# Kernel optimization log

Measured on AMD Instinct MI355X. Metric: run time of the kernel, lower is better.

## Reference

```python
import jax, jax.numpy as jnp
import numpy as np


def _log_g(x):
    # numerically stable log of g(x) = where(x>=0, x+0.5, sigmoid(x))
    return jnp.where(x >= 0, jnp.log(jax.nn.relu(x) + 0.5), -jax.nn.softplus(-x))


def setup_inputs() -> dict:
    key = jax.random.key(0)
    k1, k2, k3, k4 = jax.random.split(key, 4)
    B, T, D = 4, 4096, 1024
    Di = 2 * D  # dim_inner = int(dim * expansion_factor), expansion_factor = 2.0
    x = jax.random.normal(k1, (B, T, D), dtype=jnp.float32)
    prev_hidden = jax.random.uniform(k2, (B, Di), dtype=jnp.float32)  # positive carry state
    # torch Linear(dim, 2*dim_inner, bias=False): stored here pre-transposed as [D, 2*Di]
    W_hg = jax.random.normal(k3, (D, 2 * Di), dtype=jnp.float32) * (1.0 / np.sqrt(D))
    # out_proj Linear(dim_inner, dim, bias=False): stored pre-transposed as [Di, D]
    W_out = jax.random.normal(k4, (Di, D), dtype=jnp.float32) * (1.0 / np.sqrt(Di))
    return {"x": x, "prev_hidden": prev_hidden, "W_hg": W_hg, "W_out": W_out}


def reference(x, prev_hidden, W_hg, W_out):
    # x: [B, T, D]; prev_hidden: [B, Di] (positive)
    T = x.shape[1]
    hg = jnp.einsum('btd,de->bte', x, W_hg)          # [B, T, 2*Di]
    hidden, gate = jnp.split(hg, 2, axis=-1)          # each [B, T, Di]

    # Heinsen log-space affine scan: h_t = (1 - z_t) * h_{t-1} + z_t * g(hidden_t)
    log_coeffs = -jax.nn.softplus(gate)               # log(1 - sigmoid(gate))
    log_values = -jax.nn.softplus(-gate) + _log_g(hidden)  # log(sigmoid(gate)) + log g(hidden)

    # prepend carry state
    prev_log = jnp.clip(jnp.log(jnp.clip(prev_hidden, 1e-8, None)), -30.0, None)[:, None]  # [B,1,Di]
    log_values = jnp.concatenate([prev_log, log_values], axis=1)      # [B, T+1, Di]
    log_coeffs = jnp.pad(log_coeffs, ((0, 0), (1, 0), (0, 0)))        # [B, T+1, Di]

    a_star = jnp.cumsum(log_coeffs, axis=1)
    h = jnp.exp(a_star + jax.lax.cumlogsumexp(log_values - a_star, axis=1))  # [B, T+1, Di]
    h = h[:, -T:]                                     # drop carry slot

    next_hidden = h[:, -1]                            # [B, Di]
    out = jnp.einsum('bte,ed->btd', h, W_out)         # [B, T, D]
    return (out, next_hidden)
```

## Files before the change

### kernel.cpp

```cpp
#include <hip/hip_runtime.h>
#include <cstdio>

#define T_LEN 4096
#define B_SZ  4
#define D_IN  1024
#define DI    2048
#define MM    16384
#define NC2   128
#define CHL2  32

typedef __attribute__((ext_vector_type(8))) __bf16 bf16x8;
typedef __attribute__((ext_vector_type(4))) float  f32x4;
typedef __attribute__((ext_vector_type(8))) unsigned short u16x8;

__device__ __forceinline__ unsigned short f2bf(float f){
  unsigned u = __builtin_bit_cast(unsigned, f);
  u += 0x7fffu + ((u >> 16) & 1u);
  return (unsigned short)(u >> 16);
}
__device__ __forceinline__ float bf2f_lo(unsigned u){
  return __builtin_bit_cast(float, u << 16);
}
__device__ __forceinline__ float bf2f_hi(unsigned u){
  return __builtin_bit_cast(float, u & 0xffff0000u);
}
__device__ __forceinline__ float bf2f_s(unsigned short s){
  return __builtin_bit_cast(float, (unsigned)s << 16);
}

__device__ __forceinline__ void async16(void* lds, const void* g){
  __builtin_amdgcn_global_load_lds((const __attribute__((address_space(1))) void*)g,
                                   (__attribute__((address_space(3))) void*)lds, 16, 0, 0);
}

template<int PERM>
__device__ __forceinline__ void transpose_body(const float* __restrict__ src,
                                               unsigned short* __restrict__ dst,
                                               int n0, int k0, int SK, int SN,
                                               float (*tile)[65], int tid){
  #pragma unroll
  for(int it=0; it<16; it++){
    int idx = it*256 + tid;
    int kk = idx>>6, nn = idx&63;
    int n = n0+nn;
    int col = PERM ? (((n>>5)<<4) + (n&15) + ((n&16)?2048:0)) : n;
    tile[kk][nn] = src[(size_t)(k0+kk)*SN + col];
  }
  __syncthreads();
  #pragma unroll
  for(int it=0; it<16; it++){
    int idx = it*256 + tid;
    int nn = idx>>6, kk = idx&63;
    dst[(size_t)(n0+nn)*SK + k0+kk] = f2bf(tile[kk][nn]);
  }
}

__global__ __launch_bounds__(256) void k_prep(const float* __restrict__ x,
                                              unsigned short* __restrict__ xb,
                                              const float* __restrict__ Whg,
                                              unsigned short* __restrict__ wt,
                                              const float* __restrict__ Wout,
                                              unsigned short* __restrict__ wo){
  __shared__ float tile[64][65];
  int bid = blockIdx.x, tid = threadIdx.x;
  if(bid < 8192){
    size_t t = (size_t)bid*256 + tid;
    const float4* xi = (const float4*)x;
    float4 a = xi[2*t], b = xi[2*t+1];
    u16x8 o;
    o[0]=f2bf(a.x); o[1]=f2bf(a.y); o[2]=f2bf(a.z); o[3]=f2bf(a.w);
    o[4]=f2bf(b.x); o[5]=f2bf(b.y); o[6]=f2bf(b.z); o[7]=f2bf(b.w);
    ((u16x8*)xb)[t] = o;
  } else if(bid < 9216){
    int j = bid - 8192;
    transpose_body<1>(Whg, wt, (j&63)*64, (j>>6)*64, 1024, 4096, tile, tid);
  } else {
    int j = bid - 9216;
    transpose_body<0>(Wout, wo, (j&15)*64, (j>>4)*64, 2048, 1024, tile, tid);
  }
}

template<int EPI>
__global__ __launch_bounds__(256, 2)
void k_gemm(const unsigned short* __restrict__ A, const unsigned short* __restrict__ Bt,
            float* __restrict__ C0, unsigned* __restrict__ U0,
            unsigned* __restrict__ U1, unsigned short* __restrict__ Ap,
            unsigned short* __restrict__ Vp, int M, int N, int K){
  __shared__ unsigned short lsA[128*64];
  __shared__ unsigned short lsB[128*64];
  int tid  = threadIdx.x;
  int lane = tid & 63, wave = tid >> 6;
  int wm = wave >> 1, wn = wave & 1;
  int cl = lane & 15, quad = lane >> 4;
  int m0 = blockIdx.y * 128, n0 = blockIdx.x * 128;

  f32x4 acc[4][4];
  #pragma unroll
  for(int i=0;i<4;i++)
    #pragma unroll
    for(int j=0;j<4;j++) acc[i][j] = (f32x4){0.f,0.f,0.f,0.f};

  int g = (tid&7) ^ ((tid>>3)&7);
  const unsigned short* gA = A  + (size_t)(m0 + (tid>>3))*K + g*8;
  const unsigned short* gB = Bt + (size_t)(n0 + (tid>>3))*K + g*8;
  unsigned short* dA = lsA + tid*8;
  unsigned short* dB = lsB + tid*8;

  for(int k0=0; k0<K; k0+=64){
    #pragma unroll
    for(int it=0; it<4; it++){
      async16(dA + it*2048, gA + (size_t)(it*32)*K + k0);
      async16(dB + it*2048, gB + (size_t)(it*32)*K + k0);
    }
    __syncthreads();
    #pragma unroll
    for(int kh=0; kh<2; kh++){
      bf16x8 fa[4], fb[4];
      int sl = ((kh<<2)|quad);
      #pragma unroll
      for(int t2=0;t2<4;t2++){
        int ra = wm*64 + t2*16 + cl;
        int rb = wn*64 + t2*16 + cl;
        fa[t2] = *(const bf16x8*)&lsA[ra*64 + (sl^(cl&7))*8];
        fb[t2] = *(const bf16x8*)&lsB[rb*64 + (sl^(cl&7))*8];
      }
      #pragma unroll
      for(int i=0;i<4;i++)
        #pragma unroll
        for(int j=0;j<4;j++)
          acc[i][j] = __builtin_amdgcn_mfma_f32_16x16x32_bf16(fa[i], fb[j], acc[i][j], 0, 0, 0);
    }
    __syncthreads();
  }

  if(EPI==0){
    #pragma unroll
    for(int i=0;i<4;i++)
      #pragma unroll
      for(int j=0;j<4;j++){
        int n = n0 + wn*64 + j*16 + cl;
        #pragma unroll
        for(int r=0;r<4;r++){
          int m = m0 + wm*64 + i*16 + quad*4 + r;
          C0[(size_t)m*N + n] = acc[i][j][r];
        }
      }
  } else {
    float* lA_f = (float*)lsA;
    float* lV_f = (float*)lsB;
    int ibase = ((n0 + wn*64) >> 1) + cl;
    int odd = cl & 1;
    #pragma unroll
    for(int i=0;i<4;i++)
      #pragma unroll
      for(int p=0;p<2;p++){
        f32x4 hh = acc[i][2*p], gg = acc[i][2*p+1];
        int ii = ibase + p*16;
        float pa = 1.f, pv = 0.f;
        #pragma unroll
        for(int r=0;r<4;r++){
          int m = m0 + wm*64 + i*16 + quad*4 + r;
          float gate = gg[r], hid = hh[r];
          float e  = __expf(gate);
          float cc = 1.f/(1.f + e);
          float z  = (gate > 80.f) ? 1.f : e*cc;
          float gv = (hid >= 0.f) ? (hid + 0.5f) : (1.f/(1.f + __expf(-hid)));
          float vv = z*gv;
          float ccp = __shfl_xor(cc, 1, 64);
          float vvp = __shfl_xor(vv, 1, 64);
          unsigned wlo = odd ? (unsigned)f2bf(vvp) : (unsigned)f2bf(cc);
          unsigned whi = odd ? (unsigned)f2bf(vv)  : (unsigned)f2bf(ccp);
          unsigned* dst = odd ? U1 : U0;
          dst[((size_t)m*DI + (ii & ~1)) >> 1] = wlo | (whi << 16);
          pa *= cc;
          pv = fmaf(cc, pv, vv);
        }
        int seg = wm*16 + i*4 + quad;
        int chl = wn*32 + p*16 + cl;
        lA_f[seg*64 + chl] = pa;
        lV_f[seg*64 + chl] = pv;
      }
    __syncthreads();
    {
      int ch = tid & 63, q = tid >> 6;
      float Ac = 1.f, Vc = 0.f;
      #pragma unroll
      for(int s=0; s<8; s++){
        int idx = (q*8 + s)*64 + ch;
        float a = lA_f[idx], v = lV_f[idx];
        Ac *= a;
        Vc = fmaf(a, Vc, v);
      }
      int b = m0 >> 12;
      int ch32 = ((m0 & 4095) >> 5) + q;
      size_t o = (size_t)(b*NC2 + ch32)*DI + (n0 >> 1) + ch;
      Ap[o] = f2bf(Ac); Vp[o] = f2bf(Vc);
    }
  }
}

__global__ __launch_bounds__(256) void k_scanB(const float* __restrict__ prev,
                                               unsigned short* __restrict__ Ap,
                                               const unsigned short* __restrict__ Vp){
  int t = blockIdx.x*256 + threadIdx.x;
  int i = t & (DI-1); int b = t >> 11;
  float h = fmaxf(prev[t], 1e-8f);
  for(int ch=0; ch<NC2; ch++){
    size_t o = (size_t)(b*NC2 + ch)*DI + i;
    float a = bf2f_s(Ap[o]), vv = bf2f_s(Vp[o]);
    Ap[o] = f2bf(h);
    h = fmaf(a, h, vv);
  }
}

__global__ __launch_bounds__(256) void k_scanC(const unsigned* __restrict__ cp,
                                               unsigned* __restrict__ vp,
                                               const unsigned* __restrict__ hinp,
                                               float* __restrict__ nh){
  int t = blockIdx.x*256 + threadIdx.x;
  int i2 = t & (DI/2 - 1);
  int ch = (t >> 10) & (NC2-1);
  int b  = t >> 17;
  size_t base = ((size_t)(b*T_LEN + ch*CHL2))*(DI/2) + i2;
  unsigned hp = hinp[(size_t)(b*NC2 + ch)*(DI/2) + i2];
  float h0 = bf2f_lo(hp), h1 = bf2f_hi(hp);
  #pragma unroll 4
  for(int s=0; s<CHL2; s++){
    unsigned cu = cp[base], vu = vp[base];
    h0 = fmaf(bf2f_lo(cu), h0, bf2f_lo(vu));
    h1 = fmaf(bf2f_hi(cu), h1, bf2f_hi(vu));
    vp[base] = (unsigned)f2bf(h0) | ((unsigned)f2bf(h1) << 16);
    base += DI/2;
  }
  if(ch == NC2-1){ nh[b*DI + 2*i2] = h0; nh[b*DI + 2*i2 + 1] = h1; }
}

extern "C" void kernel_launch(void* const* d_in, const int* in_sizes, int n_in,
                              void* d_out, int out_size, void* d_ws, size_t ws_size,
                              hipStream_t stream){
  const float* x    = (const float*)d_in[0];
  const float* prev = (const float*)d_in[1];
  const float* Whg  = (const float*)d_in[2];
  const float* Wout = (const float*)d_in[3];
  float* out = (float*)d_out;
  float* nh  = out + (size_t)MM*D_IN;

  const size_t NEED = 117440512;
  if(ws_size < NEED){
    fprintf(stderr, "kernel_launch: ws_size=%zu < needed %zu — aborting launch\n",
            ws_size, NEED);
    return;
  }
  char* ws = (char*)d_ws;
  unsigned short* xb = (unsigned short*)(ws);
  unsigned short* wt = (unsigned short*)(ws + 33554432);
  unsigned short* wo = (unsigned short*)(ws + 41943040);
  unsigned short* v  = (unsigned short*)(ws + 46137344);
  unsigned short* Ap = (unsigned short*)(ws + 113246208);
  unsigned short* Vp = (unsigned short*)(ws + 115343360);
  unsigned* c = (unsigned*)d_out;

  k_prep<<<9728, 256, 0, stream>>>(x, xb, Whg, wt, Wout, wo);

  k_gemm<1><<<dim3(32,128), 256, 0, stream>>>(xb, wt, nullptr, c, (unsigned*)v,
                                              Ap, Vp, MM, 2*DI, D_IN);

  k_scanB<<<32,   256, 0, stream>>>(prev, Ap, Vp);
  k_scanC<<<2048, 256, 0, stream>>>((const unsigned*)c, (unsigned*)v,
                                    (const unsigned*)Ap, nh);

  k_gemm<0><<<dim3(8,128), 256, 0, stream>>>(v, wo, out, nullptr, nullptr,
                                             nullptr, nullptr, MM, D_IN, DI);
}
```

Before: 422.4 us.

## Rewrite GEMM with 256x256 tiles, 4-stage async LDS pipeline and block swizzle

The bf16 MFMA GEMM moves from 128x128 tiles with 256 threads and a single-buffered K=64 loop to 256x256 tiles with 512 threads. K advances in steps of 32 through a 4-deep ring of LDS buffers, with loads issued three stages ahead and guarded by manual vmcnt waits and barriers. It also remaps workgroups for L2 locality and raises wave priority around the MFMA bursts. The aim is to hide global-load latency and raise data reuse. The costs are much more LDS per block, more registers for the accumulators, which can limit occupancy, and fragile hand-written synchronisation.

```diff
diff --git a/kernel.cpp b/kernel.cpp
--- a/kernel.cpp
+++ b/kernel.cpp
@@ -32,6 +32,9 @@
   __builtin_amdgcn_global_load_lds((const __attribute__((address_space(1))) void*)g,
                                    (__attribute__((address_space(3))) void*)lds, 16, 0, 0);
 }
+
+#define BARRIER()    asm volatile("s_barrier" ::: "memory")
+#define VMCNT_BAR(n) asm volatile("s_waitcnt vmcnt(" #n ")\n\ts_barrier" ::: "memory")
 
 template<int PERM>
 __device__ __forceinline__ void transpose_body(const float* __restrict__ src,
@@ -81,68 +84,110 @@
 }
 
 template<int EPI>
-__global__ __launch_bounds__(256, 2)
+__global__ __launch_bounds__(512, 2)
 void k_gemm(const unsigned short* __restrict__ A, const unsigned short* __restrict__ Bt,
             float* __restrict__ C0, unsigned* __restrict__ U0,
             unsigned* __restrict__ U1, unsigned short* __restrict__ Ap,
             unsigned short* __restrict__ Vp, int M, int N, int K){
-  __shared__ unsigned short lsA[128*64];
-  __shared__ unsigned short lsB[128*64];
+  __shared__ __align__(16) unsigned short lsA[4*8192];
+  __shared__ __align__(16) unsigned short lsB[4*8192];
   int tid  = threadIdx.x;
   int lane = tid & 63, wave = tid >> 6;
-  int wm = wave >> 1, wn = wave & 1;
+  int wm = wave >> 2, wn = wave & 3;
   int cl = lane & 15, quad = lane >> 4;
-  int m0 = blockIdx.y * 128, n0 = blockIdx.x * 128;
-
-  f32x4 acc[4][4];
+
+  int gx = gridDim.x;
+  int nwg = gx * gridDim.y;
+  int orig = blockIdx.y * gx + blockIdx.x;
+  int swz = (orig & 7) * (nwg >> 3) + (orig >> 3);
+  int bx = swz % gx, by = swz / gx;
+  int m0 = by * 256, n0 = bx * 256;
+
+  f32x4 acc[8][4];
   #pragma unroll
-  for(int i=0;i<4;i++)
+  for(int i=0;i<8;i++)
     #pragma unroll
     for(int j=0;j<4;j++) acc[i][j] = (f32x4){0.f,0.f,0.f,0.f};
 
-  int g = (tid&7) ^ ((tid>>3)&7);
-  const unsigned short* gA = A  + (size_t)(m0 + (tid>>3))*K + g*8;
-  const unsigned short* gB = Bt + (size_t)(n0 + (tid>>3))*K + g*8;
-  unsigned short* dA = lsA + tid*8;
-  unsigned short* dB = lsB + tid*8;
-
-  for(int k0=0; k0<K; k0+=64){
-    #pragma unroll
-    for(int it=0; it<4; it++){
-      async16(dA + it*2048, gA + (size_t)(it*32)*K + k0);
-      async16(dB + it*2048, gB + (size_t)(it*32)*K + k0);
+  const unsigned short* gA = A  + (size_t)(m0 + (tid>>2))*K + (tid&3)*8;
+  const unsigned short* gB = Bt + (size_t)(n0 + (tid>>2))*K + (tid&3)*8;
+  unsigned short* dA0 = lsA + tid*8;
+  unsigned short* dB0 = lsB + tid*8;
+  const size_t rK = (size_t)128*K;
+
+  int NU = K >> 5;
+
+  #pragma unroll
+  for(int w0=0; w0<3; ++w0){
+    int sw = w0*8192;
+    async16(dA0 + sw,        gA + (size_t)w0*32);
+    async16(dA0 + sw + 4096, gA + rK + (size_t)w0*32);
+    async16(dB0 + sw,        gB + (size_t)w0*32);
+    async16(dB0 + sw + 4096, gB + rK + (size_t)w0*32);
+  }
+  VMCNT_BAR(8);
+
+  for(int u=0; u<NU; ++u){
+    const unsigned short* sA = lsA + (u&3)*8192 + wm*128*32;
+    const unsigned short* sB = lsB + (u&3)*8192 + wn*64*32;
+    int w = u + 3;
+    bool st = w < NU;
+    int sw = (w&3)*8192;
+
+    bf16x8 fb[4], fa[4];
+    #pragma unroll
+    for(int nf=0; nf<4; nf++)
+      fb[nf] = *(const bf16x8*)&sB[(nf*16+cl)*32 + quad*8];
+    #pragma unroll
+    for(int mf=0; mf<4; mf++)
+      fa[mf] = *(const bf16x8*)&sA[(mf*16+cl)*32 + quad*8];
+    if(st){
+      async16(dA0 + sw, gA + (size_t)w*32);
+      async16(dB0 + sw, gB + (size_t)w*32);
     }
-    __syncthreads();
-    #pragma unroll
-    for(int kh=0; kh<2; kh++){
-      bf16x8 fa[4], fb[4];
-      int sl = ((kh<<2)|quad);
-      #pragma unroll
-      for(int t2=0;t2<4;t2++){
-        int ra = wm*64 + t2*16 + cl;
-        int rb = wn*64 + t2*16 + cl;
-        fa[t2] = *(const bf16x8*)&lsA[ra*64 + (sl^(cl&7))*8];
-        fb[t2] = *(const bf16x8*)&lsB[rb*64 + (sl^(cl&7))*8];
-      }
-      #pragma unroll
-      for(int i=0;i<4;i++)
+    BARRIER();
+    __builtin_amdgcn_s_setprio(1);
+    #pragma unroll
+    for(int mf=0; mf<4; mf++)
+      #pragma unroll
+      for(int nf=0; nf<4; nf++)
+        acc[mf][nf] = __builtin_amdgcn_mfma_f32_16x16x32_bf16(fa[mf], fb[nf], acc[mf][nf], 0,0,0);
+    __builtin_amdgcn_s_setprio(0);
+    BARRIER();
+
+    #pragma unroll
+    for(int mf=0; mf<4; mf++)
+      fa[mf] = *(const bf16x8*)&sA[((mf+4)*16+cl)*32 + quad*8];
+    if(st){
+      async16(dA0 + sw + 4096, gA + rK + (size_t)w*32);
+      async16(dB0 + sw + 4096, gB + rK + (size_t)w*32);
+    }
+    BARRIER();
+    __builtin_amdgcn_s_setprio(1);
+    #pragma unroll
+    for(int mf=0; mf<4; mf++)
+      #pragma unroll
+      for(int nf=0; nf<4; nf++)
+        acc[mf+4][nf] = __builtin_amdgcn_mfma_f32_16x16x32_bf16(fa[mf], fb[nf], acc[mf+4][nf], 0,0,0);
+    __builtin_amdgcn_s_setprio(0);
+
+    int rem = NU - 1 - u;
+    if(rem >= 3)      VMCNT_BAR(8);
+    else if(rem == 2) VMCNT_BAR(4);
+    else if(rem == 1) VMCNT_BAR(0);
+    else              BARRIER();
+  }
+
+  if(EPI==0){
+    #pragma unroll
+    for(int mf=0; mf<8; mf++)
+      #pragma unroll
+      for(int nf=0; nf<4; nf++){
+        int n = n0 + wn*64 + nf*16 + cl;
         #pragma unroll
-        for(int j=0;j<4;j++)
-          acc[i][j] = __builtin_amdgcn_mfma_f32_16x16x32_bf16(fa[i], fb[j], acc[i][j], 0, 0, 0);
-    }
-    __syncthreads();
-  }
-
-  if(EPI==0){
-    #pragma unroll
-    for(int i=0;i<4;i++)
-      #pragma unroll
-      for(int j=0;j<4;j++){
-        int n = n0 + wn*64 + j*16 + cl;
-        #pragma unroll
-        for(int r=0;r<4;r++){
-          int m = m0 + wm*64 + i*16 + quad*4 + r;
-          C0[(size_t)m*N + n] = acc[i][j][r];
+        for(int r=0; r<4; r++){
+          int m = m0 + wm*128 + mf*16 + quad*4 + r;
+          C0[(size_t)m*N + n] = acc[mf][nf][r];
         }
       }
   } else {
@@ -151,15 +196,15 @@
     int ibase = ((n0 + wn*64) >> 1) + cl;
     int odd = cl & 1;
     #pragma unroll
-    for(int i=0;i<4;i++)
-      #pragma unroll
-      for(int p=0;p<2;p++){
-        f32x4 hh = acc[i][2*p], gg = acc[i][2*p+1];
+    for(int mf=0; mf<8; mf++)
+      #pragma unroll
+      for(int p=0; p<2; p++){
+        f32x4 hh = acc[mf][2*p], gg = acc[mf][2*p+1];
         int ii = ibase + p*16;
         float pa = 1.f, pv = 0.f;
         #pragma unroll
-        for(int r=0;r<4;r++){
-          int m = m0 + wm*64 + i*16 + quad*4 + r;
+        for(int r=0; r<4; r++){
+          int m = m0 + wm*128 + mf*16 + quad*4 + r;
           float gate = gg[r], hid = hh[r];
           float e  = __expf(gate);
           float cc = 1.f/(1.f + e);
@@ -175,26 +220,30 @@
           pa *= cc;
           pv = fmaf(cc, pv, vv);
         }
-        int seg = wm*16 + i*4 + quad;
+        int seg = wm*32 + mf*4 + quad;
         int chl = wn*32 + p*16 + cl;
-        lA_f[seg*64 + chl] = pa;
-        lV_f[seg*64 + chl] = pv;
+        lA_f[seg*128 + chl] = pa;
+        lV_f[seg*128 + chl] = pv;
       }
     __syncthreads();
     {
-      int ch = tid & 63, q = tid >> 6;
-      float Ac = 1.f, Vc = 0.f;
-      #pragma unroll
-      for(int s=0; s<8; s++){
-        int idx = (q*8 + s)*64 + ch;
-        float a = lA_f[idx], v = lV_f[idx];
-        Ac *= a;
-        Vc = fmaf(a, Vc, v);
+      int chl = tid & 127;
+      int b = m0 >> 12;
+      #pragma unroll
+      for(int qq=0; qq<2; qq++){
+        int q = (tid >> 7) + qq*4;
+        float Ac = 1.f, Vc = 0.f;
+        #pragma unroll
+        for(int s=0; s<8; s++){
+          int idx = (q*8 + s)*128 + chl;
+          float a = lA_f[idx], v = lV_f[idx];
+          Ac *= a;
+          Vc = fmaf(a, Vc, v);
+        }
+        int ch32 = ((m0 & 4095) >> 5) + q;
+        size_t o = (size_t)(b*NC2 + ch32)*DI + (n0 >> 1) + chl;
+        Ap[o] = f2bf(Ac); Vp[o] = f2bf(Vc);
       }
-      int b = m0 >> 12;
-      int ch32 = ((m0 & 4095) >> 5) + q;
-      size_t o = (size_t)(b*NC2 + ch32)*DI + (n0 >> 1) + ch;
-      Ap[o] = f2bf(Ac); Vp[o] = f2bf(Vc);
     }
   }
 }
@@ -262,13 +311,13 @@
 
   k_prep<<<9728, 256, 0, stream>>>(x, xb, Whg, wt, Wout, wo);
 
-  k_gemm<1><<<dim3(32,128), 256, 0, stream>>>(xb, wt, nullptr, c, (unsigned*)v,
-                                              Ap, Vp, MM, 2*DI, D_IN);
+  k_gemm<1><<<dim3(16,64), 512, 0, stream>>>(xb, wt, nullptr, c, (unsigned*)v,
+                                             Ap, Vp, MM, 2*DI, D_IN);
 
   k_scanB<<<32,   256, 0, stream>>>(prev, Ap, Vp);
   k_scanC<<<2048, 256, 0, stream>>>((const unsigned*)c, (unsigned*)v,
                                     (const unsigned*)Ap, nh);
 
-  k_gemm<0><<<dim3(8,128), 256, 0, stream>>>(v, wo, out, nullptr, nullptr,
-                                             nullptr, nullptr, MM, D_IN, DI);
-}
+  k_gemm<0><<<dim3(4,64), 512, 0, stream>>>(v, wo, out, nullptr, nullptr,
+                                            nullptr, nullptr, MM, D_IN, DI);
+}
```

Result: slower. 433.3 us (+2.6%).
